# Performance work log

Hardware: AMD Instinct MI355X
Metric: run time of the kernel (lower is better)

Reference implementation:

```python
import jax, jax.numpy as jnp
import numpy as np
from jax import lax

P = 2048
HIDDEN = 512
NUM_STEPS = 15
BATCH = 8192
SLOPE = 25.0  # snntorch surrogate.fast_sigmoid default slope


@jax.custom_vjp
def spike_fn(x):
    # Heaviside forward, fast-sigmoid surrogate backward.
    return (x > 0).astype(x.dtype)

def _spike_fwd(x):
    return spike_fn(x), x

def _spike_bwd(x, g):
    return (g / (SLOPE * jnp.abs(x) + 1.0) ** 2,)

spike_fn.defvjp(_spike_fwd, _spike_bwd)


def setup_inputs() -> dict:
    key = jax.random.key(0)
    ks = jax.random.split(key, 6)
    x = jax.random.randint(ks[0], (BATCH, 2), 0, P)
    embed = jax.random.normal(ks[1], (P, HIDDEN), dtype=jnp.float32)
    # Linear weights stored [in, out] (transpose of torch convention, same math)
    W1 = jax.random.normal(ks[2], (2 * HIDDEN, HIDDEN), dtype=jnp.float32) * (1.0 / np.sqrt(2 * HIDDEN))
    b1 = jnp.zeros((HIDDEN,), dtype=jnp.float32)
    W2 = jax.random.normal(ks[3], (HIDDEN, P), dtype=jnp.float32) * (1.0 / np.sqrt(HIDDEN))
    b2 = jnp.zeros((P,), dtype=jnp.float32)
    beta1 = jnp.float32(0.9)
    thr1 = jnp.float32(1.0)
    beta2 = jnp.float32(0.9)
    thr2 = jnp.float32(1.0)
    return {"x": x, "embed": embed, "W1": W1, "b1": b1, "W2": W2, "b2": b2,
            "beta1": beta1, "thr1": thr1, "beta2": beta2, "thr2": thr2}


def reference(x, embed, W1, b1, W2, b2, beta1, thr1, beta2, thr2):
    # clamp params as in the torch no-grad block (identity at init values)
    beta1 = jnp.clip(beta1, 0.1, 0.9)
    beta2 = jnp.clip(beta2, 0.1, 0.9)
    thr1 = jnp.clip(thr1, 0.1, None)
    thr2 = jnp.clip(thr2, 0.1, None)

    emb = embed[x].reshape(x.shape[0], -1)          # [B, 2*hidden]
    cur1 = emb @ W1 + b1                            # constant across steps

    mem1_0 = jnp.zeros((x.shape[0], HIDDEN), dtype=jnp.float32)
    mem2_0 = jnp.zeros((x.shape[0], P), dtype=jnp.float32)

    def step(carry, _):
        mem1, mem2 = carry
        # snntorch Leaky, reset_mechanism='subtract': reset from PREVIOUS mem, detached
        reset1 = lax.stop_gradient((mem1 - thr1 > 0).astype(mem1.dtype))
        mem1 = beta1 * mem1 + cur1 - reset1 * thr1
        spk1 = spike_fn(mem1 - thr1)
        cur2 = spk1 @ W2 + b2
        # lif2 has reset_mechanism='none'
        mem2 = beta2 * mem2 + cur2
        return (mem1, mem2), None

    (mem1, mem2), _ = lax.scan(step, (mem1_0, mem2_0), None, length=NUM_STEPS)
    return mem2  # output = last mem2
```

## Files before the change

### kernel.cpp

```cpp
#include <hip/hip_runtime.h>
#include <hip/hip_bf16.h>
#include <stdint.h>

typedef float    f32x4 __attribute__((ext_vector_type(4)));
typedef _Float16 f16x4 __attribute__((ext_vector_type(4)));
typedef _Float16 f16x8 __attribute__((ext_vector_type(8)));

#define NSTEPS 15

__global__ __launch_bounds__(256) void prep_kernel(
    const float* __restrict__ embed, const float* __restrict__ W1,
    const float* __restrict__ W2, const float* __restrict__ b2,
    const float* __restrict__ beta2p,
    _Float16* __restrict__ Ap, _Float16* __restrict__ Btp,
    _Float16* __restrict__ W2T, float* __restrict__ bias2s)
{
  __shared__ _Float16 sh[2][64][72];
  const int b = blockIdx.x;
  const int t = threadIdx.x;

  if (b < 1024) {
    const int i  = b * 256 + t;
    const int m  = i >> 7;
    const int k4 = (i & 127) * 4;
    f32x4 v = *(const f32x4*)&embed[(size_t)m * 512 + k4];
    f16x4 h0, h1;
#pragma unroll
    for (int j = 0; j < 4; ++j) {
      h0[j] = (_Float16)v[j];
      h1[j] = (_Float16)(v[j] - (float)h0[j]);
    }
    _Float16* r = Ap + (size_t)m * 1536 + k4;
    *(f16x4*)(r)        = h0;
    *(f16x4*)(r + 512)  = h1;
    *(f16x4*)(r + 1024) = h0;
  } else if (b < 1152) {
    const int idx = b - 1024;
    const int n0 = (idx & 7) * 64;
    const int k0 = ((idx >> 3) & 7) * 64;
    const int z  = idx >> 6;
    const int kk = t >> 4;
    const int n4 = (t & 15) * 4;
#pragma unroll
    for (int i = 0; i < 4; ++i) {
      f32x4 v = *(const f32x4*)&W1[(size_t)(z * 512 + k0 + kk + i * 16) * 512 + n0 + n4];
#pragma unroll
      for (int j = 0; j < 4; ++j) {
        float s = v[j] * 64.0f;
        _Float16 hi = (_Float16)s;
        sh[0][n4 + j][kk + i * 16] = hi;
        sh[1][n4 + j][kk + i * 16] = (_Float16)(s - (float)hi);
      }
    }
    __syncthreads();
#pragma unroll
    for (int i = 0; i < 2; ++i) {
      const int nn = (t >> 3) + i * 32;
      const int k8 = (t & 7) * 8;
      _Float16* r = Btp + (size_t)(z * 512 + n0 + nn) * 1536 + k0 + k8;
      uint4 h = *(const uint4*)&sh[0][nn][k8];
      *(uint4*)(r)        = h;
      *(uint4*)(r + 512)  = h;
      *(uint4*)(r + 1024) = *(const uint4*)&sh[1][nn][k8];
    }
  } else if (b < 1408) {
    const int idx = b - 1152;
    const int n0 = (idx & 31) * 64;
    const int k0 = (idx >> 5) * 64;
    const int kk = t >> 4;
    const int n4 = (t & 15) * 4;
#pragma unroll
    for (int i = 0; i < 4; ++i) {
      f32x4 v = *(const f32x4*)&W2[(size_t)(k0 + kk + i * 16) * 2048 + n0 + n4];
#pragma unroll
      for (int j = 0; j < 4; ++j) sh[0][n4 + j][kk + i * 16] = (_Float16)v[j];
    }
    __syncthreads();
#pragma unroll
    for (int i = 0; i < 2; ++i) {
      const int nn = (t >> 3) + i * 32;
      const int k8 = (t & 7) * 8;
      *(uint4*)&W2T[(size_t)(n0 + nn) * 512 + k0 + k8] = *(const uint4*)&sh[0][nn][k8];
    }
  } else {
    const float beta2 = fminf(fmaxf(beta2p[0], 0.1f), 0.9f);
    float cb = 0.0f;
    for (int i = 0; i < NSTEPS; ++i) cb = beta2 * cb + 1.0f;
    const int n = (b - 1408) * 256 + t;
    if (n < 2048) bias2s[n] = cb * b2[n];
  }
}

__global__ __launch_bounds__(256) void recur_kernel(
    const int* __restrict__ x,
    const float* __restrict__ T,
    const float* __restrict__ b1,
    const float* __restrict__ beta1p, const float* __restrict__ thr1p,
    const float* __restrict__ beta2p,
    _Float16* __restrict__ S)
{
  const float beta1 = fminf(fmaxf(beta1p[0], 0.1f), 0.9f);
  const float thr1  = fmaxf(thr1p[0], 0.1f);
  const float beta2 = fminf(fmaxf(beta2p[0], 0.1f), 0.9f);

  const int t = threadIdx.x;
  const int b = blockIdx.x * 4 + (t >> 6);
  const int h = (t & 63) * 8;
  const int x0 = x[b * 2 + 0];
  const int x1 = x[b * 2 + 1];

  const float* t0 = &T[(size_t)x0 * 1024 + h];
  const float* t1 = &T[(size_t)x1 * 1024 + 512 + h];

  float cur[8];
  {
    f32x4 a0 = *(const f32x4*)(t0);
    f32x4 a1 = *(const f32x4*)(t0 + 4);
    f32x4 c0 = *(const f32x4*)(t1);
    f32x4 c1 = *(const f32x4*)(t1 + 4);
    f32x4 e0 = *(const f32x4*)&b1[h];
    f32x4 e1 = *(const f32x4*)&b1[h + 4];
#pragma unroll
    for (int j = 0; j < 4; ++j) {
      cur[j]     = a0[j] + c0[j] + e0[j];
      cur[4 + j] = a1[j] + c1[j] + e1[j];
    }
  }

  float m[8] = {}, s[8] = {};
#pragma unroll
  for (int st = 0; st < NSTEPS; ++st) {
#pragma unroll
    for (int j = 0; j < 8; ++j) {
      float r = (m[j] > thr1) ? thr1 : 0.0f;
      m[j] = beta1 * m[j] + cur[j] - r;
      float sp = (m[j] > thr1) ? 1.0f : 0.0f;
      s[j] = beta2 * s[j] + sp;
    }
  }

  __align__(16) _Float16 o[8];
#pragma unroll
  for (int j = 0; j < 8; ++j) o[j] = (_Float16)s[j];
  *(uint4*)&S[(size_t)b * 512 + h] = *(const uint4*)o;
}

__device__ __forceinline__ void gld_lds16(const void* g, void* l) {
  __builtin_amdgcn_global_load_lds(
      (const __attribute__((address_space(1))) uint32_t*)g,
      (__attribute__((address_space(3))) uint32_t*)l, 16, 0, 0);
}

template<int BM, int BN, int WM_, int WN_, int LDA, int LDB, int LDC,
         int KTILES, int NTN, bool BIAS>
__global__ __launch_bounds__(256) void mfma_gemm_kernel(
    const _Float16* __restrict__ A, const _Float16* __restrict__ Bt,
    const float* __restrict__ bias, float* __restrict__ C, float scale)
{
  constexpr int FM  = BM / (WM_ * 16);
  constexpr int FN  = BN / (WN_ * 16);
  constexpr int ITA = BM / 32;
  constexpr int ITB = BN / 32;

  __shared__ __align__(16) char lds[BM * 128 + BN * 128];
  char* AsB = lds;
  char* BsB = lds + BM * 128;

  const int t    = threadIdx.x;
  const int lane = t & 63;
  const int wave = t >> 6;
  const int wm   = wave / WN_;
  const int wn   = wave % WN_;

  int bid = blockIdx.x;
  bid = (bid & 7) * (gridDim.x >> 3) + (bid >> 3);
  const int m0 = (bid / NTN) * BM;
  const int n0 = (bid % NTN) * BN;

  f32x4 acc[FM][FN] = {};

  for (int kt = 0; kt < KTILES; ++kt) {
    const int k0 = kt * 64;
#pragma unroll
    for (int i = 0; i < ITA; ++i) {
      const int ob  = i * 4096 + wave * 1024;
      const int o   = ob + lane * 16;
      const int row = o >> 7;
      const int c   = ((o >> 4) & 7) ^ (row & 7);
      gld_lds16(A + ((size_t)(m0 + row) * LDA + k0 + c * 8), AsB + ob);
    }
#pragma unroll
    for (int i = 0; i < ITB; ++i) {
      const int ob  = i * 4096 + wave * 1024;
      const int o   = ob + lane * 16;
      const int row = o >> 7;
      const int c   = ((o >> 4) & 7) ^ (row & 7);
      gld_lds16(Bt + ((size_t)(n0 + row) * LDB + k0 + c * 8), BsB + ob);
    }
    asm volatile("s_waitcnt vmcnt(0)" ::: "memory");
    __syncthreads();

#pragma unroll
    for (int kk = 0; kk < 2; ++kk) {
      const int lc = (lane >> 4) + kk * 4;
      f16x8 af[FM], bf[FN];
#pragma unroll
      for (int mi = 0; mi < FM; ++mi) {
        const int row = wm * (FM * 16) + mi * 16 + (lane & 15);
        af[mi] = *(const f16x8*)(AsB + row * 128 + ((lc ^ (row & 7)) << 4));
      }
#pragma unroll
      for (int ni = 0; ni < FN; ++ni) {
        const int row = wn * (FN * 16) + ni * 16 + (lane & 15);
        bf[ni] = *(const f16x8*)(BsB + row * 128 + ((lc ^ (row & 7)) << 4));
      }
#pragma unroll
      for (int mi = 0; mi < FM; ++mi)
#pragma unroll
        for (int ni = 0; ni < FN; ++ni)
          acc[mi][ni] = __builtin_amdgcn_mfma_f32_16x16x32_f16(
              af[mi], bf[ni], acc[mi][ni], 0, 0, 0);
    }
    __syncthreads();
  }

#pragma unroll
  for (int mi = 0; mi < FM; ++mi) {
    const int r0 = m0 + wm * (FM * 16) + mi * 16 + ((lane >> 4) << 2);
#pragma unroll
    for (int ni = 0; ni < FN; ++ni) {
      const int cc = n0 + wn * (FN * 16) + ni * 16 + (lane & 15);
      const float bv = BIAS ? bias[cc] : 0.0f;
#pragma unroll
      for (int q = 0; q < 4; ++q)
        C[(size_t)(r0 + q) * LDC + cc] = acc[mi][ni][q] * scale + bv;
    }
  }
}

extern "C" void kernel_launch(void* const* d_in, const int* in_sizes, int n_in,
                              void* d_out, int out_size, void* d_ws, size_t ws_size,
                              hipStream_t stream) {
  const int*   x     = (const int*)  d_in[0];
  const float* embed = (const float*)d_in[1];
  const float* W1    = (const float*)d_in[2];
  const float* b1    = (const float*)d_in[3];
  const float* W2    = (const float*)d_in[4];
  const float* b2    = (const float*)d_in[5];
  const float* beta1 = (const float*)d_in[6];
  const float* thr1  = (const float*)d_in[7];
  const float* beta2 = (const float*)d_in[8];
  float* out = (float*)d_out;

  char* ws = (char*)d_ws;
  _Float16* Ap     = (_Float16*)ws;
  _Float16* Btp    = (_Float16*)(ws + ( 6u << 20));
  float*    T      = (float*)   (ws + ( 9u << 20));
  _Float16* W2T    = (_Float16*)(ws + (17u << 20));
  _Float16* S      = (_Float16*)(ws + (19u << 20));
  float*    bias2s = (float*)   (ws + (27u << 20));

  prep_kernel<<<dim3(1416), 256, 0, stream>>>(embed, W1, W2, b2, beta2,
                                              Ap, Btp, W2T, bias2s);

  mfma_gemm_kernel<128, 64, 4, 1, 1536, 1536, 1024, 24, 16, false>
      <<<dim3(256), 256, 0, stream>>>(Ap, Btp, nullptr, T, 1.0f / 64.0f);

  recur_kernel<<<dim3(2048), 256, 0, stream>>>(x, T, b1, beta1, thr1, beta2, S);

  mfma_gemm_kernel<128, 128, 2, 2, 512, 512, 2048, 8, 16, true>
      <<<dim3(1024), 256, 0, stream>>>(S, W2T, bias2s, out, 1.0f);
}
```

Measured before the change: 71.93 us.

## Split first GEMM's K dimension across two blocks and drop duplicated operand copies

The first GEMM (embedding-table times W1 with a hi/lo fp16 split) now runs on a 256x2 grid. Each z-slice handles half of the 1536-long virtual K range and writes its own partial result, and the recurrence kernel adds the two partials when it gathers. The Ap and Btp operands no longer store the third duplicated K segment; column indices are remapped inside the new kernel instead. This doubles the number of blocks to fill the GPU better and cuts prep writes. In exchange it doubles the T buffer traffic and adds extra gathers in the recurrence kernel.

```diff
diff --git a/kernel.cpp b/kernel.cpp
--- a/kernel.cpp
+++ b/kernel.cpp
@@ -30,10 +30,9 @@
       h0[j] = (_Float16)v[j];
       h1[j] = (_Float16)(v[j] - (float)h0[j]);
     }
-    _Float16* r = Ap + (size_t)m * 1536 + k4;
-    *(f16x4*)(r)        = h0;
-    *(f16x4*)(r + 512)  = h1;
-    *(f16x4*)(r + 1024) = h0;
+    _Float16* r = Ap + (size_t)m * 1024 + k4;
+    *(f16x4*)(r)       = h0;
+    *(f16x4*)(r + 512) = h1;
   } else if (b < 1152) {
     const int idx = b - 1024;
     const int n0 = (idx & 7) * 64;
@@ -57,11 +56,9 @@
     for (int i = 0; i < 2; ++i) {
       const int nn = (t >> 3) + i * 32;
       const int k8 = (t & 7) * 8;
-      _Float16* r = Btp + (size_t)(z * 512 + n0 + nn) * 1536 + k0 + k8;
-      uint4 h = *(const uint4*)&sh[0][nn][k8];
-      *(uint4*)(r)        = h;
-      *(uint4*)(r + 512)  = h;
-      *(uint4*)(r + 1024) = *(const uint4*)&sh[1][nn][k8];
+      _Float16* r = Btp + (size_t)(z * 512 + n0 + nn) * 1024 + k0 + k8;
+      *(uint4*)(r)       = *(const uint4*)&sh[0][nn][k8];
+      *(uint4*)(r + 512) = *(const uint4*)&sh[1][nn][k8];
     }
   } else if (b < 1408) {
     const int idx = b - 1152;
@@ -91,9 +88,97 @@
   }
 }
 
+__device__ __forceinline__ void gld_lds16(const void* g, void* l) {
+  __builtin_amdgcn_global_load_lds(
+      (const __attribute__((address_space(1))) uint32_t*)g,
+      (__attribute__((address_space(3))) uint32_t*)l, 16, 0, 0);
+}
+
+__global__ __launch_bounds__(256) void gemm1_kernel(
+    const _Float16* __restrict__ Ap,
+    const _Float16* __restrict__ Btp,
+    float* __restrict__ Tp)
+{
+  __shared__ __align__(16) char lds[(128 + 64) * 128];
+  char* AsB = lds;
+  char* BsB = lds + 128 * 128;
+
+  const int t    = threadIdx.x;
+  const int lane = t & 63;
+  const int wave = t >> 6;
+  const int z    = blockIdx.y;
+
+  int bid = blockIdx.x;
+  bid = (bid & 7) * 32 + (bid >> 3);
+  const int m0 = (bid >> 4) * 128;
+  const int n0 = (bid & 15) * 64;
+
+  f32x4 acc[2][4] = {};
+
+  for (int kt = 0; kt < 12; ++kt) {
+    const int k0   = z * 768 + kt * 64;
+    const int acol = (k0 < 1024) ? k0 : k0 - 1024;
+    const int bcol = (k0 < 1024) ? (k0 & 511) : k0 - 512;
+#pragma unroll
+    for (int i = 0; i < 4; ++i) {
+      const int ob  = i * 4096 + wave * 1024;
+      const int o   = ob + lane * 16;
+      const int row = o >> 7;
+      const int c   = ((o >> 4) & 7) ^ (row & 7);
+      gld_lds16(Ap + ((size_t)(m0 + row) * 1024 + acol + c * 8), AsB + ob);
+    }
+#pragma unroll
+    for (int i = 0; i < 2; ++i) {
+      const int ob  = i * 4096 + wave * 1024;
+      const int o   = ob + lane * 16;
+      const int row = o >> 7;
+      const int c   = ((o >> 4) & 7) ^ (row & 7);
+      gld_lds16(Btp + ((size_t)(n0 + row) * 1024 + bcol + c * 8), BsB + ob);
+    }
+    asm volatile("s_waitcnt vmcnt(0)" ::: "memory");
+    __syncthreads();
+
+#pragma unroll
+    for (int kk = 0; kk < 2; ++kk) {
+      const int lc = (lane >> 4) + kk * 4;
+      f16x8 af[2], bf[4];
+#pragma unroll
+      for (int mi = 0; mi < 2; ++mi) {
+        const int row = wave * 32 + mi * 16 + (lane & 15);
+        af[mi] = *(const f16x8*)(AsB + row * 128 + ((lc ^ (row & 7)) << 4));
+      }
+#pragma unroll
+      for (int ni = 0; ni < 4; ++ni) {
+        const int row = ni * 16 + (lane & 15);
+        bf[ni] = *(const f16x8*)(BsB + row * 128 + ((lc ^ (row & 7)) << 4));
+      }
+#pragma unroll
+      for (int mi = 0; mi < 2; ++mi)
+#pragma unroll
+        for (int ni = 0; ni < 4; ++ni)
+          acc[mi][ni] = __builtin_amdgcn_mfma_f32_16x16x32_f16(
+              af[mi], bf[ni], acc[mi][ni], 0, 0, 0);
+    }
+    __syncthreads();
+  }
+
+  float* Cz = Tp + (size_t)z * 2048 * 1024;
+#pragma unroll
+  for (int mi = 0; mi < 2; ++mi) {
+    const int r0 = m0 + wave * 32 + mi * 16 + ((lane >> 4) << 2);
+#pragma unroll
+    for (int ni = 0; ni < 4; ++ni) {
+      const int cc = n0 + ni * 16 + (lane & 15);
+#pragma unroll
+      for (int q = 0; q < 4; ++q)
+        Cz[(size_t)(r0 + q) * 1024 + cc] = acc[mi][ni][q] * 0.015625f;
+    }
+  }
+}
+
 __global__ __launch_bounds__(256) void recur_kernel(
     const int* __restrict__ x,
-    const float* __restrict__ T,
+    const float* __restrict__ Tp,
     const float* __restrict__ b1,
     const float* __restrict__ beta1p, const float* __restrict__ thr1p,
     const float* __restrict__ beta2p,
@@ -102,6 +187,7 @@
   const float beta1 = fminf(fmaxf(beta1p[0], 0.1f), 0.9f);
   const float thr1  = fmaxf(thr1p[0], 0.1f);
   const float beta2 = fminf(fmaxf(beta2p[0], 0.1f), 0.9f);
+  const size_t ZS = (size_t)2048 * 1024;
 
   const int t = threadIdx.x;
   const int b = blockIdx.x * 4 + (t >> 6);
@@ -109,22 +195,20 @@
   const int x0 = x[b * 2 + 0];
   const int x1 = x[b * 2 + 1];
 
-  const float* t0 = &T[(size_t)x0 * 1024 + h];
-  const float* t1 = &T[(size_t)x1 * 1024 + 512 + h];
+  const float* p00 = &Tp[(size_t)x0 * 1024 + h];
+  const float* p01 = &Tp[(size_t)x1 * 1024 + 512 + h];
 
   float cur[8];
-  {
-    f32x4 a0 = *(const f32x4*)(t0);
-    f32x4 a1 = *(const f32x4*)(t0 + 4);
-    f32x4 c0 = *(const f32x4*)(t1);
-    f32x4 c1 = *(const f32x4*)(t1 + 4);
-    f32x4 e0 = *(const f32x4*)&b1[h];
-    f32x4 e1 = *(const f32x4*)&b1[h + 4];
-#pragma unroll
-    for (int j = 0; j < 4; ++j) {
-      cur[j]     = a0[j] + c0[j] + e0[j];
-      cur[4 + j] = a1[j] + c1[j] + e1[j];
-    }
+#pragma unroll
+  for (int half = 0; half < 2; ++half) {
+    f32x4 a0 = *(const f32x4*)(p00 + half * 4);
+    f32x4 a1 = *(const f32x4*)(p00 + ZS + half * 4);
+    f32x4 c0 = *(const f32x4*)(p01 + half * 4);
+    f32x4 c1 = *(const f32x4*)(p01 + ZS + half * 4);
+    f32x4 e  = *(const f32x4*)&b1[h + half * 4];
+#pragma unroll
+    for (int j = 0; j < 4; ++j)
+      cur[half * 4 + j] = (a0[j] + a1[j]) + (c0[j] + c1[j]) + e[j];
   }
 
   float m[8] = {}, s[8] = {};
@@ -143,12 +227,6 @@
 #pragma unroll
   for (int j = 0; j < 8; ++j) o[j] = (_Float16)s[j];
   *(uint4*)&S[(size_t)b * 512 + h] = *(const uint4*)o;
-}
-
-__device__ __forceinline__ void gld_lds16(const void* g, void* l) {
-  __builtin_amdgcn_global_load_lds(
-      (const __attribute__((address_space(1))) uint32_t*)g,
-      (__attribute__((address_space(3))) uint32_t*)l, 16, 0, 0);
 }
 
 template<int BM, int BN, int WM_, int WN_, int LDA, int LDB, int LDC,
@@ -253,20 +331,19 @@
   float* out = (float*)d_out;
 
   char* ws = (char*)d_ws;
-  _Float16* Ap     = (_Float16*)ws;
-  _Float16* Btp    = (_Float16*)(ws + ( 6u << 20));
-  float*    T      = (float*)   (ws + ( 9u << 20));
-  _Float16* W2T    = (_Float16*)(ws + (17u << 20));
-  _Float16* S      = (_Float16*)(ws + (19u << 20));
-  float*    bias2s = (float*)   (ws + (27u << 20));
+  float*    Tp     = (float*)   ws;
+  _Float16* Ap     = (_Float16*)(ws + (16u << 20));
+  _Float16* Btp    = (_Float16*)(ws + (20u << 20));
+  _Float16* W2T    = (_Float16*)(ws + (22u << 20));
+  _Float16* S      = (_Float16*)(ws + (24u << 20));
+  float*    bias2s = (float*)   (ws + (32u << 20));
 
   prep_kernel<<<dim3(1416), 256, 0, stream>>>(embed, W1, W2, b2, beta2,
                                               Ap, Btp, W2T, bias2s);
 
-  mfma_gemm_kernel<128, 64, 4, 1, 1536, 1536, 1024, 24, 16, false>
-      <<<dim3(256), 256, 0, stream>>>(Ap, Btp, nullptr, T, 1.0f / 64.0f);
-
-  recur_kernel<<<dim3(2048), 256, 0, stream>>>(x, T, b1, beta1, thr1, beta2, S);
+  gemm1_kernel<<<dim3(256, 2), 256, 0, stream>>>(Ap, Btp, Tp);
+
+  recur_kernel<<<dim3(2048), 256, 0, stream>>>(x, Tp, b1, beta1, thr1, beta2, S);
 
   mfma_gemm_kernel<128, 128, 2, 2, 512, 512, 2048, 8, 16, true>
       <<<dim3(1024), 256, 0, stream>>>(S, W2T, bias2s, out, 1.0f);
```

After: 65.71 us. 1.09x faster.
